# Performance work log

Hardware: AMD Instinct MI355X
Metric: run time of the kernel (lower is better)

Reference implementation:

```python
import jax, jax.numpy as jnp
import numpy as np

N_A, N_P, E = 50000, 50000, 600000
H, D = 8, 16
C = H * D  # hidden_channels = 128
OUT = 16
F_A, F_P = 256, 128
NEG_SLOPE = 0.2
EPS = 1e-5


def setup_inputs():
    key = jax.random.key(0)
    ks = jax.random.split(key, 16)
    return {
        'x_author': jax.random.normal(ks[0], (N_A, F_A), jnp.float32),
        'x_paper': jax.random.normal(ks[1], (N_P, F_P), jnp.float32),
        'W_a': jax.random.normal(ks[2], (F_A, C), jnp.float32) / np.sqrt(F_A).astype(np.float32),
        'b_a': jnp.zeros((C,), jnp.float32),
        'W_p': jax.random.normal(ks[3], (F_P, C), jnp.float32) / np.sqrt(F_P).astype(np.float32),
        'b_p': jnp.zeros((C,), jnp.float32),
        'att_src_ap': jax.random.normal(ks[4], (H, D), jnp.float32) * 0.1,
        'att_dst_ap': jax.random.normal(ks[5], (H, D), jnp.float32) * 0.1,
        'att_src_pp': jax.random.normal(ks[6], (H, D), jnp.float32) * 0.1,
        'att_dst_pp': jax.random.normal(ks[7], (H, D), jnp.float32) * 0.1,
        'k_W': jax.random.normal(ks[8], (C, C), jnp.float32) / np.sqrt(C).astype(np.float32),
        'k_b': jnp.zeros((C,), jnp.float32),
        'q': jax.random.normal(ks[9], (C,), jnp.float32) * 0.1,
        'norm_w': jnp.ones((C,), jnp.float32),
        'norm_b': jnp.zeros((C,), jnp.float32),
        'norm_ms': jnp.ones((C,), jnp.float32),
        'lin_W': jax.random.normal(ks[10], (C, OUT), jnp.float32) / np.sqrt(C).astype(np.float32),
        'lin_b': jnp.zeros((OUT,), jnp.float32),
        'edge_ap': jax.random.randint(ks[11], (2, E), 0, N_A),
        'edge_pp': jax.random.randint(ks[12], (2, E), 0, N_P),
    }


def _edge_type_out(h_src, h_dst, edge, a_src, a_dst, n_dst):
    # Node-level attention for one edge type (PyG HANConv per-metapath GAT).
    alpha_s = jnp.einsum('nhd,hd->nh', h_src, a_src)  # [N_src, H]
    alpha_d = jnp.einsum('nhd,hd->nh', h_dst, a_dst)  # [N_dst, H]
    src, dst = edge[0], edge[1]
    alpha = alpha_s[src] + alpha_d[dst]                       # [E, H]
    alpha = jnp.where(alpha >= 0, alpha, NEG_SLOPE * alpha)   # leaky_relu(0.2)
    m = jax.ops.segment_max(alpha, dst, num_segments=n_dst)
    e = jnp.exp(alpha - m[dst])
    denom = jax.ops.segment_sum(e, dst, num_segments=n_dst)
    attn = e / denom[dst]                                     # softmax over incoming edges
    msg = h_src[src] * attn[:, :, None]                       # [E, H, D]
    out = jax.ops.segment_sum(msg, dst, num_segments=n_dst)   # [n_dst, H, D]
    return jax.nn.relu(out.reshape(n_dst, H * D))


def reference(x_author, x_paper, W_a, b_a, W_p, b_p, att_src_ap, att_dst_ap,
              att_src_pp, att_dst_pp, k_W, k_b, q, norm_w, norm_b, norm_ms,
              lin_W, lin_b, edge_ap, edge_pp):
    # per-node-type projections -> [N, H, D]
    h_a = (x_author @ W_a + b_a).reshape(N_A, H, D)
    h_p = (x_paper @ W_p + b_p).reshape(N_P, H, D)
    # per-edge-type node-level attention + aggregation (both target 'paper')
    out_ap = _edge_type_out(h_a, h_p, edge_ap, att_src_ap, att_dst_ap, N_P)
    out_pp = _edge_type_out(h_p, h_p, edge_pp, att_src_pp, att_dst_pp, N_P)
    # semantic-level attention across the R=2 meta-paths
    outs = jnp.stack([out_ap, out_pp], axis=0)               # [R, N_P, C]
    w = jnp.tanh(outs @ k_W + k_b).mean(axis=1) @ q          # [R]
    beta = jax.nn.softmax(w)
    out = jnp.einsum('rnc,r->nc', outs, beta)                # [N_P, C]
    # GraphNorm (single graph: stats over all nodes)
    mean = out.mean(axis=0)
    o = out - mean * norm_ms
    var = (o * o).mean(axis=0)
    o = norm_w * o / jnp.sqrt(var + EPS) + norm_b
    # final classifier
    return o @ lin_W + lin_b
```

## Files before the change

### kernel.cpp

```cpp
#include <hip/hip_runtime.h>
#include <math.h>

#define NN   50000
#define EE   600000
#define CCH  128
#define HH   8
#define DD   16
#define OUTC 16
#define NEG  0.2f
#define EPSN 1e-5f
#define SLICE_DIV 12500
#define CHUNKS 1172
#define CAP 64

typedef _Float16 f16x8 __attribute__((ext_vector_type(8)));
typedef float    f32x4 __attribute__((ext_vector_type(4)));

__device__ __forceinline__ float fast_tanh(float x) {
    x = fminf(10.f, fmaxf(-10.f, x));
    float e = __expf(2.f * x);
    return (e - 1.f) / (e + 1.f);
}

__global__ __launch_bounds__(256) void convw_k(const float* __restrict__ W_a,
        const float* __restrict__ W_p, const float* __restrict__ k_W,
        const float* __restrict__ lin_W, _Float16* __restrict__ Wt_a,
        _Float16* __restrict__ Wt_p, _Float16* __restrict__ kWt,
        _Float16* __restrict__ linWt)
{
    int id = blockIdx.x * 256 + threadIdx.x;
    if (id < 32768) {
        int k = id >> 7, n = id & 127;
        Wt_a[n * 256 + k] = (_Float16)W_a[id];
    } else if (id < 49152) {
        int i = id - 32768; int k = i >> 7, n = i & 127;
        Wt_p[n * 128 + k] = (_Float16)W_p[i];
    } else if (id < 65536) {
        int i = id - 49152; int k = i >> 7, n = i & 127;
        kWt[n * 128 + k] = (_Float16)k_W[i];
    } else if (id < 67584) {
        int i = id - 65536; int k = i >> 4, n = i & 15;
        linWt[n * 128 + k] = (_Float16)lin_W[i];
    }
}

__global__ __launch_bounds__(256) void gemm2h_k(const float* __restrict__ X_a,
        const float* __restrict__ X_p, const _Float16* __restrict__ Wt_a,
        const _Float16* __restrict__ Wt_p, const float* __restrict__ b_a,
        const float* __restrict__ b_p,
        const float* __restrict__ att_s_ap, const float* __restrict__ att_d_ap,
        const float* __restrict__ att_s_pp, const float* __restrict__ att_d_pp,
        _Float16* __restrict__ h_a, _Float16* __restrict__ h_p,
        float* __restrict__ as_ap, float* __restrict__ ad_ap,
        float* __restrict__ as_pp, float* __restrict__ ad_pp,
        const int* __restrict__ ea, const int* __restrict__ ep,
        int* __restrict__ fill, int* __restrict__ csrp, int GBn)
{
    __shared__ _Float16 As[64][40];
    __shared__ _Float16 Bs[128][40];
    const int t = threadIdx.x;
    if ((int)blockIdx.x >= 2 * GBn) {
        int bb = (int)blockIdx.x - 2 * GBn;
        int slice = bb & 7;
        int chunk = bb >> 3;
        int lo = slice * SLICE_DIV, hi = lo + SLICE_DIV;
        int base = chunk * 1024;
#pragma unroll
        for (int it = 0; it < 4; ++it) {
            int e = base + it * 256 + t;
            if (e < EE) {
                int d = ea[EE + e];
                if (d >= lo && d < hi) {
                    int pos = atomicAdd(&fill[d], 1);
                    if (pos < CAP) csrp[(size_t)d * CAP + pos] = ea[e];
                }
            } else if (e < 2 * EE) {
                int d = NN + ep[e];
                if (d >= lo && d < hi) {
                    int pos = atomicAdd(&fill[d], 1);
                    if (pos < CAP) csrp[(size_t)d * CAP + pos] = ep[e - EE];
                }
            }
        }
        return;
    }
    const int which = ((int)blockIdx.x >= GBn) ? 1 : 0;
    const float* X = which ? X_p : X_a;
    const _Float16* Wt = which ? Wt_p : Wt_a;
    const float* bias = which ? b_p : b_a;
    _Float16* Y = which ? h_p : h_a;
    const int K = which ? 128 : 256;
    const int r0 = (blockIdx.x - which * GBn) * 64;
    const int lane = t & 63;
    const int wv = t >> 6;
    const int m16 = lane & 15;
    const int kq = lane >> 4;
    f32x4 acc[8];
#pragma unroll
    for (int i = 0; i < 8; ++i) acc[i] = (f32x4){0.f, 0.f, 0.f, 0.f};

    const int ar = t >> 2;
    const int ak = (t & 3) * 8;
    const int br = t >> 1;
    const int bk = (t & 1) * 16;

    for (int kc = 0; kc < K; kc += 32) {
        int row = r0 + ar;
        f16x8 av;
        if (row < NN) {
            const float4* gp = (const float4*)&X[row * K + kc + ak];
            float4 x0 = gp[0], x1 = gp[1];
            av[0] = (_Float16)x0.x; av[1] = (_Float16)x0.y;
            av[2] = (_Float16)x0.z; av[3] = (_Float16)x0.w;
            av[4] = (_Float16)x1.x; av[5] = (_Float16)x1.y;
            av[6] = (_Float16)x1.z; av[7] = (_Float16)x1.w;
        } else {
#pragma unroll
            for (int j = 0; j < 8; ++j) av[j] = (_Float16)0.f;
        }
        *(f16x8*)&As[ar][ak] = av;
        const f16x8* wp = (const f16x8*)&Wt[br * K + kc + bk];
        *(f16x8*)&Bs[br][bk]     = wp[0];
        *(f16x8*)&Bs[br][bk + 8] = wp[1];
        __syncthreads();
        f16x8 af = *(const f16x8*)&As[wv * 16 + m16][kq * 8];
#pragma unroll
        for (int i = 0; i < 8; ++i) {
            f16x8 bf = *(const f16x8*)&Bs[i * 16 + m16][kq * 8];
            acc[i] = __builtin_amdgcn_mfma_f32_16x16x32_f16(af, bf, acc[i], 0, 0, 0);
        }
        __syncthreads();
    }
    const int rbase = r0 + wv * 16 + kq * 4;
#pragma unroll
    for (int i = 0; i < 8; ++i) {
        int col = i * 16 + m16;
        float b = bias[col];
        float hv[4];
#pragma unroll
        for (int rr = 0; rr < 4; ++rr) hv[rr] = acc[i][rr] + b;
#pragma unroll
        for (int rr = 0; rr < 4; ++rr)
            if (rbase + rr < NN) Y[(rbase + rr) * 128 + col] = (_Float16)hv[rr];
        if (which == 0) {
            float av = att_s_ap[i * 16 + m16];
            float p[4];
#pragma unroll
            for (int rr = 0; rr < 4; ++rr) p[rr] = hv[rr] * av;
#pragma unroll
            for (int x = 1; x < 16; x <<= 1)
#pragma unroll
                for (int rr = 0; rr < 4; ++rr) p[rr] += __shfl_xor(p[rr], x, 64);
            if (m16 == 0) {
#pragma unroll
                for (int rr = 0; rr < 4; ++rr)
                    if (rbase + rr < NN) as_ap[(rbase + rr) * 8 + i] = p[rr];
            }
        } else {
            float a1 = att_d_ap[i * 16 + m16];
            float a2 = att_s_pp[i * 16 + m16];
            float a3 = att_d_pp[i * 16 + m16];
            float p1[4], p2[4], p3[4];
#pragma unroll
            for (int rr = 0; rr < 4; ++rr) {
                p1[rr] = hv[rr] * a1; p2[rr] = hv[rr] * a2; p3[rr] = hv[rr] * a3;
            }
#pragma unroll
            for (int x = 1; x < 16; x <<= 1) {
#pragma unroll
                for (int rr = 0; rr < 4; ++rr) {
                    p1[rr] += __shfl_xor(p1[rr], x, 64);
                    p2[rr] += __shfl_xor(p2[rr], x, 64);
                    p3[rr] += __shfl_xor(p3[rr], x, 64);
                }
            }
            if (m16 == 0) {
#pragma unroll
                for (int rr = 0; rr < 4; ++rr) {
                    if (rbase + rr < NN) {
                        ad_ap[(rbase + rr) * 8 + i] = p1[rr];
                        as_pp[(rbase + rr) * 8 + i] = p2[rr];
                        ad_pp[(rbase + rr) * 8 + i] = p3[rr];
                    }
                }
            }
        }
    }
}

__global__ __launch_bounds__(256) void agg4_k(
        const _Float16* __restrict__ h_a, const _Float16* __restrict__ h_p,
        const float* __restrict__ as_ap, const float* __restrict__ ad_ap,
        const float* __restrict__ as_pp, const float* __restrict__ ad_pp,
        const int* __restrict__ fill, const int* __restrict__ csrp,
        _Float16* __restrict__ out_ap, _Float16* __restrict__ out_pp)
{
    int wave = threadIdx.x >> 6;
    int lane = threadIdx.x & 63;
    int q = lane >> 4;
    int sub = lane & 15;
    int gnode = blockIdx.x * 16 + wave * 4 + q;
    bool pp = gnode >= NN;
    int n = pp ? gnode - NN : gnode;
    const _Float16* hsrc = pp ? h_p : h_a;
    const float* as = pp ? as_pp : as_ap;
    const float* ad = pp ? ad_pp : ad_ap;
    _Float16* outb = pp ? out_pp : out_ap;
    int h = sub >> 1;
    float adv = ad[n * 8 + h];
    int cnt = fill[gnode];
    if (cnt > CAP) cnt = CAP;
    const int* row = &csrp[(size_t)gnode * CAP];
    int p = 0, p1 = cnt;
    float l = 0.f;
    float acc[8] = {0.f, 0.f, 0.f, 0.f, 0.f, 0.f, 0.f, 0.f};
    for (; p + 3 < p1; p += 4) {
        int s0 = row[p], s1 = row[p + 1], s2 = row[p + 2], s3 = row[p + 3];
        float a0 = as[s0 * 8 + h] + adv;
        float a1 = as[s1 * 8 + h] + adv;
        float a2 = as[s2 * 8 + h] + adv;
        float a3 = as[s3 * 8 + h] + adv;
        a0 = (a0 >= 0.f) ? a0 : NEG * a0;
        a1 = (a1 >= 0.f) ? a1 : NEG * a1;
        a2 = (a2 >= 0.f) ? a2 : NEG * a2;
        a3 = (a3 >= 0.f) ? a3 : NEG * a3;
        float w0 = __expf(a0), w1 = __expf(a1), w2 = __expf(a2), w3 = __expf(a3);
        f16x8 v0 = *(const f16x8*)&hsrc[s0 * CCH + sub * 8];
        f16x8 v1 = *(const f16x8*)&hsrc[s1 * CCH + sub * 8];
        f16x8 v2 = *(const f16x8*)&hsrc[s2 * CCH + sub * 8];
        f16x8 v3 = *(const f16x8*)&hsrc[s3 * CCH + sub * 8];
        l += (w0 + w1) + (w2 + w3);
#pragma unroll
        for (int i = 0; i < 8; ++i)
            acc[i] += (w0 * (float)v0[i] + w1 * (float)v1[i])
                    + (w2 * (float)v2[i] + w3 * (float)v3[i]);
    }
    for (; p < p1; ++p) {
        int s0 = row[p];
        float a0 = as[s0 * 8 + h] + adv;
        a0 = (a0 >= 0.f) ? a0 : NEG * a0;
        float w0 = __expf(a0);
        f16x8 v0 = *(const f16x8*)&hsrc[s0 * CCH + sub * 8];
        l += w0;
#pragma unroll
        for (int i = 0; i < 8; ++i) acc[i] += w0 * (float)v0[i];
    }
    float inv = (l > 0.f) ? 1.f / l : 0.f;
    f16x8 o;
#pragma unroll
    for (int i = 0; i < 8; ++i) o[i] = (_Float16)fmaxf(acc[i] * inv, 0.f);
    *(f16x8*)&outb[n * CCH + sub * 8] = o;
}

__global__ __launch_bounds__(256) void semstats2_k(const _Float16* __restrict__ Xa,
        const _Float16* __restrict__ Xb, const _Float16* __restrict__ kWt,
        const float* __restrict__ kb, const float* __restrict__ q,
        float* __restrict__ wacc, float* __restrict__ sA, float* __restrict__ sB,
        float* __restrict__ ssA, float* __restrict__ ssB, float* __restrict__ sAB,
        int GBn)
{
    __shared__ float sbuf[640];
    const int t = threadIdx.x;
    if ((int)blockIdx.x < 256) {
        for (int i = t; i < 640; i += 256) sbuf[i] = 0.f;
        __syncthreads();
        int oct = t & 15, rs = t >> 4;
        int start = (int)blockIdx.x * 196;
        int end = start + 196; if (end > NN) end = NN;
        float sa[8] = {0,0,0,0,0,0,0,0}, sb[8] = {0,0,0,0,0,0,0,0};
        float ssa[8] = {0,0,0,0,0,0,0,0}, ssb[8] = {0,0,0,0,0,0,0,0};
        float sab[8] = {0,0,0,0,0,0,0,0};
        for (int r = start + rs; r < end; r += 16) {
            f16x8 va = *(const f16x8*)&Xa[r * 128 + oct * 8];
            f16x8 vb = *(const f16x8*)&Xb[r * 128 + oct * 8];
#pragma unroll
            for (int j = 0; j < 8; ++j) {
                float a = (float)va[j], b = (float)vb[j];
                sa[j] += a; sb[j] += b;
                ssa[j] += a * a; ssb[j] += b * b; sab[j] += a * b;
            }
        }
#pragma unroll
        for (int x = 16; x < 64; x <<= 1) {
#pragma unroll
            for (int j = 0; j < 8; ++j) {
                sa[j]  += __shfl_xor(sa[j],  x, 64);
                sb[j]  += __shfl_xor(sb[j],  x, 64);
                ssa[j] += __shfl_xor(ssa[j], x, 64);
                ssb[j] += __shfl_xor(ssb[j], x, 64);
                sab[j] += __shfl_xor(sab[j], x, 64);
            }
        }
        if ((t & 63) < 16) {
            int c0 = oct * 8;
#pragma unroll
            for (int j = 0; j < 8; ++j) {
                atomicAdd(&sbuf[c0 + j], sa[j]);
                atomicAdd(&sbuf[128 + c0 + j], sb[j]);
                atomicAdd(&sbuf[256 + c0 + j], ssa[j]);
                atomicAdd(&sbuf[384 + c0 + j], ssb[j]);
                atomicAdd(&sbuf[512 + c0 + j], sab[j]);
            }
        }
        __syncthreads();
        if (t < 128) {
            atomicAdd(&sA[t],  sbuf[t]);
            atomicAdd(&sB[t],  sbuf[128 + t]);
            atomicAdd(&ssA[t], sbuf[256 + t]);
            atomicAdd(&ssB[t], sbuf[384 + t]);
            atomicAdd(&sAB[t], sbuf[512 + t]);
        }
    } else {
        const int b = (int)blockIdx.x - 256;
        const int which = (b >= GBn) ? 1 : 0;
        const _Float16* Xh = which ? Xb : Xa;
        const int r0 = (b - which * GBn) * 64;
        const int lane = t & 63, wv = t >> 6;
        const int m16 = lane & 15, kq = lane >> 4;
        const int arow = r0 + wv * 16 + m16;
        f16x8 af[4];
        if (arow < NN) {
#pragma unroll
            for (int kc4 = 0; kc4 < 4; ++kc4)
                af[kc4] = *(const f16x8*)&Xh[arow * 128 + kc4 * 32 + kq * 8];
        } else {
#pragma unroll
            for (int kc4 = 0; kc4 < 4; ++kc4)
#pragma unroll
                for (int j = 0; j < 8; ++j) af[kc4][j] = (_Float16)0.f;
        }
        f32x4 acc[8];
#pragma unroll
        for (int i = 0; i < 8; ++i) acc[i] = (f32x4){0.f, 0.f, 0.f, 0.f};
#pragma unroll
        for (int kc4 = 0; kc4 < 4; ++kc4) {
#pragma unroll
            for (int i = 0; i < 8; ++i) {
                f16x8 bf = *(const f16x8*)&kWt[(i * 16 + m16) * 128 + kc4 * 32 + kq * 8];
                acc[i] = __builtin_amdgcn_mfma_f32_16x16x32_f16(af[kc4], bf, acc[i], 0, 0, 0);
            }
        }
        const int rbase = r0 + wv * 16 + kq * 4;
        float local = 0.f;
#pragma unroll
        for (int i = 0; i < 8; ++i) {
            float kbc = kb[i * 16 + m16], qc = q[i * 16 + m16];
#pragma unroll
            for (int rr = 0; rr < 4; ++rr)
                if (rbase + rr < NN) local += fast_tanh(acc[i][rr] + kbc) * qc;
        }
#pragma unroll
        for (int x = 1; x < 64; x <<= 1) local += __shfl_xor(local, x, 64);
        if (lane == 0) sbuf[wv] = local;
        __syncthreads();
        if (t == 0) {
            float s = sbuf[0] + sbuf[1] + sbuf[2] + sbuf[3];
            atomicAdd(&wacc[which * 256 + (b & 15) * 16], s);
        }
    }
}

__global__ __launch_bounds__(256) void final2_k(
        const _Float16* __restrict__ oa, const _Float16* __restrict__ ob,
        const float* __restrict__ wacc,
        const float* __restrict__ sA, const float* __restrict__ sB,
        const float* __restrict__ ssA, const float* __restrict__ ssB,
        const float* __restrict__ sAB,
        const float* __restrict__ ms, const float* __restrict__ nw,
        const float* __restrict__ nb,
        const _Float16* __restrict__ linWt, const float* __restrict__ linb,
        float* __restrict__ out)
{
    __shared__ _Float16 As[64][136];
    __shared__ float scl[128], shf[128];
    __shared__ float bcoef[2];
    int t = threadIdx.x;
    if (t < 128) {
        float w0s = 0.f, w1s = 0.f;
#pragma unroll
        for (int i = 0; i < 16; ++i) {
            w0s += wacc[i * 16];
            w1s += wacc[256 + i * 16];
        }
        float w0 = w0s * (1.f / NN), w1 = w1s * (1.f / NN);
        float mm = fmaxf(w0, w1);
        float e0 = __expf(w0 - mm), e1 = __expf(w1 - mm);
        float b0 = e0 / (e0 + e1), b1 = e1 / (e0 + e1);
        if (t == 0) { bcoef[0] = b0; bcoef[1] = b1; }
        int c = t;
        float mean = (b0 * sA[c] + b1 * sB[c]) * (1.f / NN);
        float ex2 = (b0 * b0 * ssA[c] + 2.f * b0 * b1 * sAB[c] + b1 * b1 * ssB[c]) * (1.f / NN);
        float a = mean * ms[c];
        float var = ex2 - 2.f * a * mean + a * a;
        float sc = nw[c] * rsqrtf(var + EPSN);
        scl[c] = sc;
        shf[c] = nb[c] - a * sc;
    }
    __syncthreads();
    float b0 = bcoef[0], b1 = bcoef[1];
    int r0 = blockIdx.x * 64;
    int row = t >> 2, cp = (t & 3) * 32;
    int gr = r0 + row;
    if (gr < NN) {
#pragma unroll
        for (int i = 0; i < 4; ++i) {
            int c0 = cp + i * 8;
            f16x8 va = *(const f16x8*)&oa[gr * CCH + c0];
            f16x8 vb = *(const f16x8*)&ob[gr * CCH + c0];
            f16x8 o;
#pragma unroll
            for (int e2 = 0; e2 < 8; ++e2) {
                float v = b0 * (float)va[e2] + b1 * (float)vb[e2];
                o[e2] = (_Float16)(v * scl[c0 + e2] + shf[c0 + e2]);
            }
            *(f16x8*)&As[row][c0] = o;
        }
    } else {
        f16x8 z;
#pragma unroll
        for (int e2 = 0; e2 < 8; ++e2) z[e2] = (_Float16)0.f;
#pragma unroll
        for (int i = 0; i < 4; ++i) *(f16x8*)&As[row][cp + i * 8] = z;
    }
    __syncthreads();
    int lane = t & 63, wv = t >> 6;
    int m16 = lane & 15, kq = lane >> 4;
    f32x4 acc = (f32x4){0.f, 0.f, 0.f, 0.f};
#pragma unroll
    for (int kc = 0; kc < 128; kc += 32) {
        f16x8 af = *(const f16x8*)&As[wv * 16 + m16][kc + kq * 8];
        f16x8 bf = *(const f16x8*)&linWt[m16 * 128 + kc + kq * 8];
        acc = __builtin_amdgcn_mfma_f32_16x16x32_f16(af, bf, acc, 0, 0, 0);
    }
    float lb = linb[m16];
#pragma unroll
    for (int r = 0; r < 4; ++r) {
        int gr2 = r0 + wv * 16 + kq * 4 + r;
        if (gr2 < NN) out[gr2 * 16 + m16] = acc[r] + lb;
    }
}

extern "C" void kernel_launch(void* const* d_in, const int* in_sizes, int n_in,
                              void* d_out, int out_size, void* d_ws, size_t ws_size,
                              hipStream_t stream) {
    const float* x_a   = (const float*)d_in[0];
    const float* x_p   = (const float*)d_in[1];
    const float* W_a   = (const float*)d_in[2];
    const float* b_a   = (const float*)d_in[3];
    const float* W_p   = (const float*)d_in[4];
    const float* b_p   = (const float*)d_in[5];
    const float* att_src_ap = (const float*)d_in[6];
    const float* att_dst_ap = (const float*)d_in[7];
    const float* att_src_pp = (const float*)d_in[8];
    const float* att_dst_pp = (const float*)d_in[9];
    const float* k_W   = (const float*)d_in[10];
    const float* k_b   = (const float*)d_in[11];
    const float* q     = (const float*)d_in[12];
    const float* norm_w = (const float*)d_in[13];
    const float* norm_b = (const float*)d_in[14];
    const float* norm_ms = (const float*)d_in[15];
    const float* lin_W = (const float*)d_in[16];
    const float* lin_b = (const float*)d_in[17];
    const int* edge_ap = (const int*)d_in[18];
    const int* edge_pp = (const int*)d_in[19];
    float* out = (float*)d_out;

    char* base = (char*)d_ws;
    size_t off = 0;
    auto alloc = [&](size_t bytes) -> void* {
        void* r = base + off;
        off += (bytes + 255) & ~(size_t)255;
        return r;
    };
    _Float16* h_a    = (_Float16*)alloc((size_t)NN * CCH * 2);
    _Float16* h_p    = (_Float16*)alloc((size_t)NN * CCH * 2);
    _Float16* out_ap = (_Float16*)alloc((size_t)NN * CCH * 2);
    _Float16* out_pp = (_Float16*)alloc((size_t)NN * CCH * 2);
    float* as_ap  = (float*)alloc((size_t)NN * HH * 4);
    float* ad_ap  = (float*)alloc((size_t)NN * HH * 4);
    float* as_pp  = (float*)alloc((size_t)NN * HH * 4);
    float* ad_pp  = (float*)alloc((size_t)NN * HH * 4);
    _Float16* Wt_a = (_Float16*)alloc((size_t)128 * 256 * 2);
    _Float16* Wt_p = (_Float16*)alloc((size_t)128 * 128 * 2);
    _Float16* kWt  = (_Float16*)alloc((size_t)128 * 128 * 2);
    _Float16* linWt = (_Float16*)alloc((size_t)16 * 128 * 2);
    int* csrp = (int*)alloc((size_t)2 * NN * CAP * 4);
    const size_t ZCOUNT = 100000 + 512 + 5 * 128;
    int* zz = (int*)alloc(ZCOUNT * 4);
    int* fill   = zz;
    float* wacc = (float*)(zz + 100000);
    float* sA   = (float*)(zz + 100512);
    float* sB   = sA + 128;
    float* ssA  = sB + 128;
    float* ssB  = ssA + 128;
    float* sAB  = ssB + 128;

    (void)in_sizes; (void)n_in; (void)out_size; (void)ws_size;

    hipMemsetAsync(zz, 0, ZCOUNT * 4, stream);

    convw_k<<<264, 256, 0, stream>>>(W_a, W_p, k_W, lin_W, Wt_a, Wt_p, kWt, linWt);

    const int GB = (NN + 63) / 64;
    gemm2h_k<<<2 * GB + CHUNKS * 8, 256, 0, stream>>>(
        x_a, x_p, Wt_a, Wt_p, b_a, b_p,
        att_src_ap, att_dst_ap, att_src_pp, att_dst_pp,
        h_a, h_p, as_ap, ad_ap, as_pp, ad_pp,
        edge_ap, edge_pp, fill, csrp, GB);

    agg4_k<<<2 * NN / 16, 256, 0, stream>>>(h_a, h_p, as_ap, ad_ap, as_pp, ad_pp,
                                            fill, csrp, out_ap, out_pp);

    semstats2_k<<<256 + 2 * GB, 256, 0, stream>>>(out_ap, out_pp, kWt, k_b, q, wacc,
                                                  sA, sB, ssA, ssB, sAB, GB);

    final2_k<<<GB, 256, 0, stream>>>(out_ap, out_pp, wacc, sA, sB, ssA, ssB, sAB,
                                     norm_ms, norm_w, norm_b, linWt, lin_b, out);
}
```

Before: 341.4 us.

## Fuse aggregation with semantic attention and GraphNorm stats; interleave scatter blocks with GEMM

Each aggregation block now handles both meta-paths for 16 paper nodes. It stages the outputs in LDS and directly computes the tanh(kW) semantic score and the per-channel sums and sums of squares. This removes the separate semstats kernel and its re-read of both output arrays. The stats atomics are spread over 32 buckets to cut contention, and final2 reduces across the buckets. The CSR scatter blocks are interleaved evenly among the GEMM blocks and each handles 8 edges per thread with the loads batched, which trades more work per block for better overlap.

```diff
diff --git a/kernel.cpp b/kernel.cpp
--- a/kernel.cpp
+++ b/kernel.cpp
@@ -10,8 +10,10 @@
 #define NEG  0.2f
 #define EPSN 1e-5f
 #define SLICE_DIV 12500
-#define CHUNKS 1172
+#define SCHUNKS 586
+#define SCATB (SCHUNKS*8)
 #define CAP 64
+#define SBKT 32
 
 typedef _Float16 f16x8 __attribute__((ext_vector_type(8)));
 typedef float    f32x4 __attribute__((ext_vector_type(4)));
@@ -59,38 +61,48 @@
     __shared__ _Float16 As[64][40];
     __shared__ _Float16 Bs[128][40];
     const int t = threadIdx.x;
-    if ((int)blockIdx.x >= 2 * GBn) {
-        int bb = (int)blockIdx.x - 2 * GBn;
+    const int G2 = 2 * GBn;
+    const int TT = G2 + SCATB;
+    const int b = (int)blockIdx.x;
+    const int hi = (int)(((long long)(b + 1) * G2) / TT);
+    const int lo = (int)(((long long)b * G2) / TT);
+    if (hi == lo) {
+        int bb = b - hi;
         int slice = bb & 7;
         int chunk = bb >> 3;
-        int lo = slice * SLICE_DIV, hi = lo + SLICE_DIV;
-        int base = chunk * 1024;
-#pragma unroll
-        for (int it = 0; it < 4; ++it) {
-            int e = base + it * 256 + t;
-            if (e < EE) {
-                int d = ea[EE + e];
-                if (d >= lo && d < hi) {
-                    int pos = atomicAdd(&fill[d], 1);
-                    if (pos < CAP) csrp[(size_t)d * CAP + pos] = ea[e];
-                }
-            } else if (e < 2 * EE) {
-                int d = NN + ep[e];
-                if (d >= lo && d < hi) {
-                    int pos = atomicAdd(&fill[d], 1);
-                    if (pos < CAP) csrp[(size_t)d * CAP + pos] = ep[e - EE];
+        int slo = slice * SLICE_DIV, shi = slo + SLICE_DIV;
+        int base = chunk * 2048 + t;
+        int d[8];
+#pragma unroll
+        for (int it = 0; it < 8; ++it) {
+            int e = base + it * 256;
+            int dd = -1;
+            if (e < EE) dd = ea[EE + e];
+            else if (e < 2 * EE) dd = NN + ep[e];
+            d[it] = dd;
+        }
+#pragma unroll
+        for (int it = 0; it < 8; ++it) {
+            int dd = d[it];
+            if (dd >= slo && dd < shi) {
+                int e = base + it * 256;
+                int pos = atomicAdd(&fill[dd], 1);
+                if (pos < CAP) {
+                    int s = (e < EE) ? ea[e] : ep[e - EE];
+                    csrp[(size_t)dd * CAP + pos] = s;
                 }
             }
         }
         return;
     }
-    const int which = ((int)blockIdx.x >= GBn) ? 1 : 0;
+    const int gb = lo;
+    const int which = (gb >= GBn) ? 1 : 0;
     const float* X = which ? X_p : X_a;
     const _Float16* Wt = which ? Wt_p : Wt_a;
     const float* bias = which ? b_p : b_a;
     _Float16* Y = which ? h_p : h_a;
     const int K = which ? 128 : 256;
-    const int r0 = (blockIdx.x - which * GBn) * 64;
+    const int r0 = (gb - which * GBn) * 64;
     const int lane = t & 63;
     const int wv = t >> 6;
     const int m16 = lane & 15;
@@ -135,10 +147,10 @@
 #pragma unroll
     for (int i = 0; i < 8; ++i) {
         int col = i * 16 + m16;
-        float b = bias[col];
+        float bv = bias[col];
         float hv[4];
 #pragma unroll
-        for (int rr = 0; rr < 4; ++rr) hv[rr] = acc[i][rr] + b;
+        for (int rr = 0; rr < 4; ++rr) hv[rr] = acc[i][rr] + bv;
 #pragma unroll
         for (int rr = 0; rr < 4; ++rr)
             if (rbase + rr < NN) Y[(rbase + rr) * 128 + col] = (_Float16)hv[rr];
@@ -188,184 +200,179 @@
     }
 }
 
-__global__ __launch_bounds__(256) void agg4_k(
+__global__ __launch_bounds__(256) void agg4f_k(
         const _Float16* __restrict__ h_a, const _Float16* __restrict__ h_p,
         const float* __restrict__ as_ap, const float* __restrict__ ad_ap,
         const float* __restrict__ as_pp, const float* __restrict__ ad_pp,
         const int* __restrict__ fill, const int* __restrict__ csrp,
-        _Float16* __restrict__ out_ap, _Float16* __restrict__ out_pp)
+        const _Float16* __restrict__ kWt, const float* __restrict__ kb,
+        const float* __restrict__ qv,
+        _Float16* __restrict__ out_ap, _Float16* __restrict__ out_pp,
+        float* __restrict__ wacc, float* __restrict__ statsb)
 {
-    int wave = threadIdx.x >> 6;
-    int lane = threadIdx.x & 63;
-    int q = lane >> 4;
-    int sub = lane & 15;
-    int gnode = blockIdx.x * 16 + wave * 4 + q;
-    bool pp = gnode >= NN;
-    int n = pp ? gnode - NN : gnode;
-    const _Float16* hsrc = pp ? h_p : h_a;
-    const float* as = pp ? as_pp : as_ap;
-    const float* ad = pp ? ad_pp : ad_ap;
-    _Float16* outb = pp ? out_pp : out_ap;
-    int h = sub >> 1;
-    float adv = ad[n * 8 + h];
-    int cnt = fill[gnode];
-    if (cnt > CAP) cnt = CAP;
-    const int* row = &csrp[(size_t)gnode * CAP];
-    int p = 0, p1 = cnt;
-    float l = 0.f;
-    float acc[8] = {0.f, 0.f, 0.f, 0.f, 0.f, 0.f, 0.f, 0.f};
-    for (; p + 3 < p1; p += 4) {
-        int s0 = row[p], s1 = row[p + 1], s2 = row[p + 2], s3 = row[p + 3];
-        float a0 = as[s0 * 8 + h] + adv;
-        float a1 = as[s1 * 8 + h] + adv;
-        float a2 = as[s2 * 8 + h] + adv;
-        float a3 = as[s3 * 8 + h] + adv;
-        a0 = (a0 >= 0.f) ? a0 : NEG * a0;
-        a1 = (a1 >= 0.f) ? a1 : NEG * a1;
-        a2 = (a2 >= 0.f) ? a2 : NEG * a2;
-        a3 = (a3 >= 0.f) ? a3 : NEG * a3;
-        float w0 = __expf(a0), w1 = __expf(a1), w2 = __expf(a2), w3 = __expf(a3);
-        f16x8 v0 = *(const f16x8*)&hsrc[s0 * CCH + sub * 8];
-        f16x8 v1 = *(const f16x8*)&hsrc[s1 * CCH + sub * 8];
-        f16x8 v2 = *(const f16x8*)&hsrc[s2 * CCH + sub * 8];
-        f16x8 v3 = *(const f16x8*)&hsrc[s3 * CCH + sub * 8];
-        l += (w0 + w1) + (w2 + w3);
-#pragma unroll
-        for (int i = 0; i < 8; ++i)
-            acc[i] += (w0 * (float)v0[i] + w1 * (float)v1[i])
-                    + (w2 * (float)v2[i] + w3 * (float)v3[i]);
-    }
-    for (; p < p1; ++p) {
-        int s0 = row[p];
-        float a0 = as[s0 * 8 + h] + adv;
-        a0 = (a0 >= 0.f) ? a0 : NEG * a0;
-        float w0 = __expf(a0);
-        f16x8 v0 = *(const f16x8*)&hsrc[s0 * CCH + sub * 8];
-        l += w0;
-#pragma unroll
-        for (int i = 0; i < 8; ++i) acc[i] += w0 * (float)v0[i];
-    }
-    float inv = (l > 0.f) ? 1.f / l : 0.f;
-    f16x8 o;
-#pragma unroll
-    for (int i = 0; i < 8; ++i) o[i] = (_Float16)fmaxf(acc[i] * inv, 0.f);
-    *(f16x8*)&outb[n * CCH + sub * 8] = o;
-}
-
-__global__ __launch_bounds__(256) void semstats2_k(const _Float16* __restrict__ Xa,
-        const _Float16* __restrict__ Xb, const _Float16* __restrict__ kWt,
-        const float* __restrict__ kb, const float* __restrict__ q,
-        float* __restrict__ wacc, float* __restrict__ sA, float* __restrict__ sB,
-        float* __restrict__ ssA, float* __restrict__ ssB, float* __restrict__ sAB,
-        int GBn)
-{
+    __shared__ _Float16 Aap[16][136];
+    __shared__ _Float16 App[16][136];
     __shared__ float sbuf[640];
+    __shared__ float wred[4];
     const int t = threadIdx.x;
-    if ((int)blockIdx.x < 256) {
-        for (int i = t; i < 640; i += 256) sbuf[i] = 0.f;
-        __syncthreads();
-        int oct = t & 15, rs = t >> 4;
-        int start = (int)blockIdx.x * 196;
-        int end = start + 196; if (end > NN) end = NN;
-        float sa[8] = {0,0,0,0,0,0,0,0}, sb[8] = {0,0,0,0,0,0,0,0};
-        float ssa[8] = {0,0,0,0,0,0,0,0}, ssb[8] = {0,0,0,0,0,0,0,0};
-        float sab[8] = {0,0,0,0,0,0,0,0};
-        for (int r = start + rs; r < end; r += 16) {
-            f16x8 va = *(const f16x8*)&Xa[r * 128 + oct * 8];
-            f16x8 vb = *(const f16x8*)&Xb[r * 128 + oct * 8];
-#pragma unroll
-            for (int j = 0; j < 8; ++j) {
-                float a = (float)va[j], b = (float)vb[j];
-                sa[j] += a; sb[j] += b;
-                ssa[j] += a * a; ssb[j] += b * b; sab[j] += a * b;
-            }
-        }
-#pragma unroll
-        for (int x = 16; x < 64; x <<= 1) {
-#pragma unroll
-            for (int j = 0; j < 8; ++j) {
-                sa[j]  += __shfl_xor(sa[j],  x, 64);
-                sb[j]  += __shfl_xor(sb[j],  x, 64);
-                ssa[j] += __shfl_xor(ssa[j], x, 64);
-                ssb[j] += __shfl_xor(ssb[j], x, 64);
-                sab[j] += __shfl_xor(sab[j], x, 64);
-            }
-        }
-        if ((t & 63) < 16) {
-            int c0 = oct * 8;
-#pragma unroll
-            for (int j = 0; j < 8; ++j) {
-                atomicAdd(&sbuf[c0 + j], sa[j]);
-                atomicAdd(&sbuf[128 + c0 + j], sb[j]);
-                atomicAdd(&sbuf[256 + c0 + j], ssa[j]);
-                atomicAdd(&sbuf[384 + c0 + j], ssb[j]);
-                atomicAdd(&sbuf[512 + c0 + j], sab[j]);
-            }
-        }
-        __syncthreads();
-        if (t < 128) {
-            atomicAdd(&sA[t],  sbuf[t]);
-            atomicAdd(&sB[t],  sbuf[128 + t]);
-            atomicAdd(&ssA[t], sbuf[256 + t]);
-            atomicAdd(&ssB[t], sbuf[384 + t]);
-            atomicAdd(&sAB[t], sbuf[512 + t]);
-        }
-    } else {
-        const int b = (int)blockIdx.x - 256;
-        const int which = (b >= GBn) ? 1 : 0;
-        const _Float16* Xh = which ? Xb : Xa;
-        const int r0 = (b - which * GBn) * 64;
-        const int lane = t & 63, wv = t >> 6;
-        const int m16 = lane & 15, kq = lane >> 4;
-        const int arow = r0 + wv * 16 + m16;
-        f16x8 af[4];
-        if (arow < NN) {
-#pragma unroll
-            for (int kc4 = 0; kc4 < 4; ++kc4)
-                af[kc4] = *(const f16x8*)&Xh[arow * 128 + kc4 * 32 + kq * 8];
-        } else {
-#pragma unroll
-            for (int kc4 = 0; kc4 < 4; ++kc4)
-#pragma unroll
-                for (int j = 0; j < 8; ++j) af[kc4][j] = (_Float16)0.f;
-        }
-        f32x4 acc[8];
-#pragma unroll
-        for (int i = 0; i < 8; ++i) acc[i] = (f32x4){0.f, 0.f, 0.f, 0.f};
-#pragma unroll
-        for (int kc4 = 0; kc4 < 4; ++kc4) {
-#pragma unroll
-            for (int i = 0; i < 8; ++i) {
-                f16x8 bf = *(const f16x8*)&kWt[(i * 16 + m16) * 128 + kc4 * 32 + kq * 8];
-                acc[i] = __builtin_amdgcn_mfma_f32_16x16x32_f16(af[kc4], bf, acc[i], 0, 0, 0);
-            }
-        }
-        const int rbase = r0 + wv * 16 + kq * 4;
-        float local = 0.f;
-#pragma unroll
-        for (int i = 0; i < 8; ++i) {
-            float kbc = kb[i * 16 + m16], qc = q[i * 16 + m16];
-#pragma unroll
-            for (int rr = 0; rr < 4; ++rr)
-                if (rbase + rr < NN) local += fast_tanh(acc[i][rr] + kbc) * qc;
-        }
-#pragma unroll
-        for (int x = 1; x < 64; x <<= 1) local += __shfl_xor(local, x, 64);
-        if (lane == 0) sbuf[wv] = local;
-        __syncthreads();
-        if (t == 0) {
-            float s = sbuf[0] + sbuf[1] + sbuf[2] + sbuf[3];
-            atomicAdd(&wacc[which * 256 + (b & 15) * 16], s);
-        }
+    const int wave = t >> 6, lane = t & 63;
+    const int q = lane >> 4, sub = lane & 15;
+    const int slot = wave * 4 + q;
+    const int n = blockIdx.x * 16 + slot;
+    const int h = sub >> 1;
+    for (int i = t; i < 640; i += 256) sbuf[i] = 0.f;
+
+    float oa[8], ob[8];
+    {
+        float adv = ad_ap[n * 8 + h];
+        int cnt = fill[n]; if (cnt > CAP) cnt = CAP;
+        const int* row = &csrp[(size_t)n * CAP];
+        int p = 0;
+        float l = 0.f;
+        float acc[8] = {0.f,0.f,0.f,0.f,0.f,0.f,0.f,0.f};
+        for (; p + 3 < cnt; p += 4) {
+            int s0 = row[p], s1 = row[p+1], s2 = row[p+2], s3 = row[p+3];
+            float a0 = as_ap[s0*8+h] + adv, a1 = as_ap[s1*8+h] + adv;
+            float a2 = as_ap[s2*8+h] + adv, a3 = as_ap[s3*8+h] + adv;
+            a0 = (a0 >= 0.f) ? a0 : NEG*a0; a1 = (a1 >= 0.f) ? a1 : NEG*a1;
+            a2 = (a2 >= 0.f) ? a2 : NEG*a2; a3 = (a3 >= 0.f) ? a3 : NEG*a3;
+            float w0 = __expf(a0), w1 = __expf(a1), w2 = __expf(a2), w3 = __expf(a3);
+            f16x8 v0 = *(const f16x8*)&h_a[s0*CCH + sub*8];
+            f16x8 v1 = *(const f16x8*)&h_a[s1*CCH + sub*8];
+            f16x8 v2 = *(const f16x8*)&h_a[s2*CCH + sub*8];
+            f16x8 v3 = *(const f16x8*)&h_a[s3*CCH + sub*8];
+            l += (w0 + w1) + (w2 + w3);
+#pragma unroll
+            for (int i = 0; i < 8; ++i)
+                acc[i] += (w0*(float)v0[i] + w1*(float)v1[i])
+                        + (w2*(float)v2[i] + w3*(float)v3[i]);
+        }
+        for (; p < cnt; ++p) {
+            int s0 = row[p];
+            float a0 = as_ap[s0*8+h] + adv;
+            a0 = (a0 >= 0.f) ? a0 : NEG*a0;
+            float w0 = __expf(a0);
+            f16x8 v0 = *(const f16x8*)&h_a[s0*CCH + sub*8];
+            l += w0;
+#pragma unroll
+            for (int i = 0; i < 8; ++i) acc[i] += w0*(float)v0[i];
+        }
+        float inv = (l > 0.f) ? 1.f/l : 0.f;
+#pragma unroll
+        for (int i = 0; i < 8; ++i) oa[i] = fmaxf(acc[i]*inv, 0.f);
+    }
+    {
+        float adv = ad_pp[n * 8 + h];
+        int cnt = fill[NN + n]; if (cnt > CAP) cnt = CAP;
+        const int* row = &csrp[(size_t)(NN + n) * CAP];
+        int p = 0;
+        float l = 0.f;
+        float acc[8] = {0.f,0.f,0.f,0.f,0.f,0.f,0.f,0.f};
+        for (; p + 3 < cnt; p += 4) {
+            int s0 = row[p], s1 = row[p+1], s2 = row[p+2], s3 = row[p+3];
+            float a0 = as_pp[s0*8+h] + adv, a1 = as_pp[s1*8+h] + adv;
+            float a2 = as_pp[s2*8+h] + adv, a3 = as_pp[s3*8+h] + adv;
+            a0 = (a0 >= 0.f) ? a0 : NEG*a0; a1 = (a1 >= 0.f) ? a1 : NEG*a1;
+            a2 = (a2 >= 0.f) ? a2 : NEG*a2; a3 = (a3 >= 0.f) ? a3 : NEG*a3;
+            float w0 = __expf(a0), w1 = __expf(a1), w2 = __expf(a2), w3 = __expf(a3);
+            f16x8 v0 = *(const f16x8*)&h_p[s0*CCH + sub*8];
+            f16x8 v1 = *(const f16x8*)&h_p[s1*CCH + sub*8];
+            f16x8 v2 = *(const f16x8*)&h_p[s2*CCH + sub*8];
+            f16x8 v3 = *(const f16x8*)&h_p[s3*CCH + sub*8];
+            l += (w0 + w1) + (w2 + w3);
+#pragma unroll
+            for (int i = 0; i < 8; ++i)
+                acc[i] += (w0*(float)v0[i] + w1*(float)v1[i])
+                        + (w2*(float)v2[i] + w3*(float)v3[i]);
+        }
+        for (; p < cnt; ++p) {
+            int s0 = row[p];
+            float a0 = as_pp[s0*8+h] + adv;
+            a0 = (a0 >= 0.f) ? a0 : NEG*a0;
+            float w0 = __expf(a0);
+            f16x8 v0 = *(const f16x8*)&h_p[s0*CCH + sub*8];
+            l += w0;
+#pragma unroll
+            for (int i = 0; i < 8; ++i) acc[i] += w0*(float)v0[i];
+        }
+        float inv = (l > 0.f) ? 1.f/l : 0.f;
+#pragma unroll
+        for (int i = 0; i < 8; ++i) ob[i] = fmaxf(acc[i]*inv, 0.f);
+    }
+    f16x8 va, vb;
+#pragma unroll
+    for (int i = 0; i < 8; ++i) { va[i] = (_Float16)oa[i]; vb[i] = (_Float16)ob[i]; }
+    *(f16x8*)&out_ap[n * CCH + sub * 8] = va;
+    *(f16x8*)&out_pp[n * CCH + sub * 8] = vb;
+    *(f16x8*)&Aap[slot][sub * 8] = va;
+    *(f16x8*)&App[slot][sub * 8] = vb;
+    float sa[8], sb[8], ssa[8], ssb[8], sab[8];
+#pragma unroll
+    for (int j = 0; j < 8; ++j) {
+        float a = oa[j], bq = ob[j];
+        sa[j] = a; sb[j] = bq; ssa[j] = a*a; ssb[j] = bq*bq; sab[j] = a*bq;
+    }
+#pragma unroll
+    for (int x = 16; x < 64; x <<= 1) {
+#pragma unroll
+        for (int j = 0; j < 8; ++j) {
+            sa[j]  += __shfl_xor(sa[j],  x, 64);
+            sb[j]  += __shfl_xor(sb[j],  x, 64);
+            ssa[j] += __shfl_xor(ssa[j], x, 64);
+            ssb[j] += __shfl_xor(ssb[j], x, 64);
+            sab[j] += __shfl_xor(sab[j], x, 64);
+        }
+    }
+    __syncthreads();
+    if (lane < 16) {
+        int c0 = sub * 8;
+#pragma unroll
+        for (int j = 0; j < 8; ++j) {
+            atomicAdd(&sbuf[c0 + j],       sa[j]);
+            atomicAdd(&sbuf[128 + c0 + j], sb[j]);
+            atomicAdd(&sbuf[256 + c0 + j], ssa[j]);
+            atomicAdd(&sbuf[384 + c0 + j], ssb[j]);
+            atomicAdd(&sbuf[512 + c0 + j], sab[j]);
+        }
+    }
+    const int m16 = lane & 15, kq = lane >> 4;
+    const int path = wave >> 1;
+    float local = 0.f;
+#pragma unroll
+    for (int j = 0; j < 4; ++j) {
+        int ct = (wave & 1) * 4 + j;
+        f32x4 acc2 = (f32x4){0.f, 0.f, 0.f, 0.f};
+#pragma unroll
+        for (int kc = 0; kc < 128; kc += 32) {
+            f16x8 af = path ? *(const f16x8*)&App[m16][kc + kq * 8]
+                            : *(const f16x8*)&Aap[m16][kc + kq * 8];
+            f16x8 bf = *(const f16x8*)&kWt[(ct * 16 + m16) * 128 + kc + kq * 8];
+            acc2 = __builtin_amdgcn_mfma_f32_16x16x32_f16(af, bf, acc2, 0, 0, 0);
+        }
+        float kbc = kb[ct * 16 + m16], qc = qv[ct * 16 + m16];
+#pragma unroll
+        for (int rr = 0; rr < 4; ++rr)
+            local += fast_tanh(acc2[rr] + kbc) * qc;
+    }
+#pragma unroll
+    for (int x = 1; x < 64; x <<= 1) local += __shfl_xor(local, x, 64);
+    if (lane == 0) wred[wave] = local;
+    __syncthreads();
+    if (t == 0) atomicAdd(&wacc[(blockIdx.x & 15) * 16],       wred[0] + wred[1]);
+    if (t == 1) atomicAdd(&wacc[256 + (blockIdx.x & 15) * 16], wred[2] + wred[3]);
+    if (t < 128) {
+        float* sp = statsb + (size_t)(blockIdx.x & (SBKT - 1)) * 128;
+        atomicAdd(&sp[t],                sbuf[t]);
+        atomicAdd(&sp[SBKT*128 + t],     sbuf[128 + t]);
+        atomicAdd(&sp[2*SBKT*128 + t],   sbuf[256 + t]);
+        atomicAdd(&sp[3*SBKT*128 + t],   sbuf[384 + t]);
+        atomicAdd(&sp[4*SBKT*128 + t],   sbuf[512 + t]);
     }
 }
 
 __global__ __launch_bounds__(256) void final2_k(
         const _Float16* __restrict__ oa, const _Float16* __restrict__ ob,
-        const float* __restrict__ wacc,
-        const float* __restrict__ sA, const float* __restrict__ sB,
-        const float* __restrict__ ssA, const float* __restrict__ ssB,
-        const float* __restrict__ sAB,
+        const float* __restrict__ wacc, const float* __restrict__ statsb,
         const float* __restrict__ ms, const float* __restrict__ nw,
         const float* __restrict__ nb,
         const _Float16* __restrict__ linWt, const float* __restrict__ linb,
@@ -388,8 +395,16 @@
         float b0 = e0 / (e0 + e1), b1 = e1 / (e0 + e1);
         if (t == 0) { bcoef[0] = b0; bcoef[1] = b1; }
         int c = t;
-        float mean = (b0 * sA[c] + b1 * sB[c]) * (1.f / NN);
-        float ex2 = (b0 * b0 * ssA[c] + 2.f * b0 * b1 * sAB[c] + b1 * b1 * ssB[c]) * (1.f / NN);
+        float vsA = 0.f, vsB = 0.f, vssA = 0.f, vssB = 0.f, vsAB = 0.f;
+        for (int i = 0; i < SBKT; ++i) {
+            vsA  += statsb[i * 128 + c];
+            vsB  += statsb[SBKT*128 + i * 128 + c];
+            vssA += statsb[2*SBKT*128 + i * 128 + c];
+            vssB += statsb[3*SBKT*128 + i * 128 + c];
+            vsAB += statsb[4*SBKT*128 + i * 128 + c];
+        }
+        float mean = (b0 * vsA + b1 * vsB) * (1.f / NN);
+        float ex2 = (b0 * b0 * vssA + 2.f * b0 * b1 * vsAB + b1 * b1 * vssB) * (1.f / NN);
         float a = mean * ms[c];
         float var = ex2 - 2.f * a * mean + a * a;
         float sc = nw[c] * rsqrtf(var + EPSN);
@@ -485,15 +500,11 @@
     _Float16* kWt  = (_Float16*)alloc((size_t)128 * 128 * 2);
     _Float16* linWt = (_Float16*)alloc((size_t)16 * 128 * 2);
     int* csrp = (int*)alloc((size_t)2 * NN * CAP * 4);
-    const size_t ZCOUNT = 100000 + 512 + 5 * 128;
+    const size_t ZCOUNT = 100000 + 512 + 5 * SBKT * 128;
     int* zz = (int*)alloc(ZCOUNT * 4);
     int* fill   = zz;
     float* wacc = (float*)(zz + 100000);
-    float* sA   = (float*)(zz + 100512);
-    float* sB   = sA + 128;
-    float* ssA  = sB + 128;
-    float* ssB  = ssA + 128;
-    float* sAB  = ssB + 128;
+    float* statsb = (float*)(zz + 100512);
 
     (void)in_sizes; (void)n_in; (void)out_size; (void)ws_size;
 
@@ -502,18 +513,16 @@
     convw_k<<<264, 256, 0, stream>>>(W_a, W_p, k_W, lin_W, Wt_a, Wt_p, kWt, linWt);
 
     const int GB = (NN + 63) / 64;
-    gemm2h_k<<<2 * GB + CHUNKS * 8, 256, 0, stream>>>(
+    gemm2h_k<<<2 * GB + SCATB, 256, 0, stream>>>(
         x_a, x_p, Wt_a, Wt_p, b_a, b_p,
         att_src_ap, att_dst_ap, att_src_pp, att_dst_pp,
         h_a, h_p, as_ap, ad_ap, as_pp, ad_pp,
         edge_ap, edge_pp, fill, csrp, GB);
 
-    agg4_k<<<2 * NN / 16, 256, 0, stream>>>(h_a, h_p, as_ap, ad_ap, as_pp, ad_pp,
-                                            fill, csrp, out_ap, out_pp);
-
-    semstats2_k<<<256 + 2 * GB, 256, 0, stream>>>(out_ap, out_pp, kWt, k_b, q, wacc,
-                                                  sA, sB, ssA, ssB, sAB, GB);
-
-    final2_k<<<GB, 256, 0, stream>>>(out_ap, out_pp, wacc, sA, sB, ssA, ssB, sAB,
+    agg4f_k<<<NN / 16, 256, 0, stream>>>(h_a, h_p, as_ap, ad_ap, as_pp, ad_pp,
+                                         fill, csrp, kWt, k_b, q,
+                                         out_ap, out_pp, wacc, statsb);
+
+    final2_k<<<GB, 256, 0, stream>>>(out_ap, out_pp, wacc, statsb,
                                      norm_ms, norm_w, norm_b, linWt, lin_b, out);
 }
```

Measured after the change: 364.3 us. +6.7%, slower.
